# Optimization experiments

Hardware: AMD Instinct MI355X
Metric: run time of the kernel (lower is better)

Reference implementation:

```python
import jax, jax.numpy as jnp
import numpy as np

IN, HID, B = 512, 512, 16384

def _linear_params(key, fan_in, fan_out, bias_const=None):
    kw, kb = jax.random.split(key)
    bound = 1.0 / np.sqrt(fan_in)
    W = jax.random.uniform(kw, (fan_out, fan_in), jnp.float32, -bound, bound)
    if bias_const is None:
        b = jax.random.uniform(kb, (fan_out,), jnp.float32, -bound, bound)
    else:
        b = jnp.full((fan_out,), bias_const, jnp.float32)
    return W, b

def setup_inputs() -> dict:
    key = jax.random.key(0)
    ks = jax.random.split(key, 11)
    x = jax.random.normal(ks[0], (B, IN), jnp.float32)
    h = jax.random.normal(ks[1], (B, HID), jnp.float32)
    c = jax.random.normal(ks[2], (B, HID), jnp.float32)
    Wxi, bxi = _linear_params(ks[3], IN, HID)
    Wxo, bxo = _linear_params(ks[4], IN, HID)
    Wxf, bxf = _linear_params(ks[5], IN, HID, bias_const=1.0)
    Wxg, bxg = _linear_params(ks[6], IN, HID)
    Whi, bhi = _linear_params(ks[7], HID, HID)
    Who, bho = _linear_params(ks[8], HID, HID)
    Whf, bhf = _linear_params(ks[9], HID, HID, bias_const=1.0)
    Whg, bhg = _linear_params(ks[10], HID, HID)
    return dict(x=x, h=h, c=c,
                Wxi=Wxi, bxi=bxi, Wxo=Wxo, bxo=bxo, Wxf=Wxf, bxf=bxf, Wxg=Wxg, bxg=bxg,
                Whi=Whi, bhi=bhi, Who=Who, bho=bho, Whf=Whf, bhf=bhf, Whg=Whg, bhg=bhg)

def reference(x, h, c,
              Wxi, bxi, Wxo, bxo, Wxf, bxf, Wxg, bxg,
              Whi, bhi, Who, bho, Whf, bhf, Whg, bhg):
    # Batch the four input projections and four hidden projections into two GEMMs.
    Wx = jnp.concatenate([Wxi, Wxg, Wxf, Wxo], axis=0)   # [4H, IN]
    Wh = jnp.concatenate([Whi, Whg, Whf, Who], axis=0)   # [4H, HID]
    bx = jnp.concatenate([bxi, bxg, bxf, bxo], axis=0)
    bh = jnp.concatenate([bhi, bhg, bhf, bho], axis=0)
    gates = x @ Wx.T + h @ Wh.T + bx + bh                 # [B, 4H]
    i_pre, g_pre, f_pre, o_pre = jnp.split(gates, 4, axis=1)
    i = jax.nn.sigmoid(i_pre)
    g = jnp.tanh(g_pre)
    f = jax.nn.sigmoid(f_pre)
    o = jax.nn.sigmoid(o_pre)
    c_new = f * c + i * g
    h_new = o * jnp.tanh(c_new)
    return (h_new, c_new)
```

## Files before the change

kernel.cpp:

```cpp
#include <hip/hip_runtime.h>
#include <cstdint>
#include <cstddef>


#define BATCH 16384
#define KDIM  1024
#define NPK   2048
#define HIDN  512

#define BM 128
#define BN 128
#define BK 32

typedef __bf16 bf16x8 __attribute__((ext_vector_type(8)));
typedef float  f32x4  __attribute__((ext_vector_type(4)));

__device__ __forceinline__ unsigned short f2bf(float f) {
  unsigned int u = __builtin_bit_cast(unsigned int, f);
  u += 0x7fffu + ((u >> 16) & 1u);
  return (unsigned short)(u >> 16);
}

__device__ __forceinline__ float fast_sigmoid(float x) {
  return __builtin_amdgcn_rcpf(1.0f + __expf(-x));
}
__device__ __forceinline__ float fast_tanh(float x) {
  return 1.0f - 2.0f * __builtin_amdgcn_rcpf(1.0f + __expf(2.0f * x));
}

__device__ __forceinline__ void gload_lds16(const void* gp, void* lds_wave_base) {
  auto g = (const __attribute__((address_space(1))) unsigned int*)(unsigned long long)gp;
  auto l = (__attribute__((address_space(3))) unsigned int*)
           (unsigned int)(unsigned long long)lds_wave_base;
  __builtin_amdgcn_global_load_lds(g, l, 16, 0, 0);
}


__global__ __launch_bounds__(256) void pack_a(const float* __restrict__ x,
                                              const float* __restrict__ h,
                                              unsigned short* __restrict__ A) {
  int c = blockIdx.x * 256 + threadIdx.x;
  int idx = c << 3;
  int b = idx >> 10;
  int k = idx & 1023;
  const float* src = (k < 512) ? (x + b * 512 + k) : (h + b * 512 + (k - 512));
  float4 lo = ((const float4*)src)[0];
  float4 hi = ((const float4*)src)[1];
  union { unsigned short s[8]; uint4 u; } o;
  o.s[0]=f2bf(lo.x); o.s[1]=f2bf(lo.y); o.s[2]=f2bf(lo.z); o.s[3]=f2bf(lo.w);
  o.s[4]=f2bf(hi.x); o.s[5]=f2bf(hi.y); o.s[6]=f2bf(hi.z); o.s[7]=f2bf(hi.w);
  ((uint4*)A)[c] = o.u;
}

struct GatePtrs {
  const float* wx[4];
  const float* wh[4];
  const float* bx[4];
  const float* bh[4];
};

__global__ __launch_bounds__(256) void pack_w(GatePtrs P,
                                              unsigned short* __restrict__ W,
                                              float* __restrict__ bias) {
  int c = blockIdx.x * 256 + threadIdx.x;
  int r = c >> 7;
  int k = (c & 127) << 3;
  int b    = r >> 7;
  int rem  = r & 127;
  int wn   = (rem >> 6) & 1;
  int gate = (rem >> 4) & 3;
  int jl   = rem & 15;
  int j = b * 32 + wn * 16 + jl;
  const float* src = (k < 512) ? (P.wx[gate] + j * 512 + k)
                               : (P.wh[gate] + j * 512 + (k - 512));
  float4 lo = ((const float4*)src)[0];
  float4 hi = ((const float4*)src)[1];
  union { unsigned short s[8]; uint4 u; } o;
  o.s[0]=f2bf(lo.x); o.s[1]=f2bf(lo.y); o.s[2]=f2bf(lo.z); o.s[3]=f2bf(lo.w);
  o.s[4]=f2bf(hi.x); o.s[5]=f2bf(hi.y); o.s[6]=f2bf(hi.z); o.s[7]=f2bf(hi.w);
  ((uint4*)W)[c] = o.u;
  if ((c & 127) == 0) bias[r] = P.bx[gate][j] + P.bh[gate][j];
}


__global__ __launch_bounds__(256) void lstm_gemm(
    const unsigned short* __restrict__ A,
    const unsigned short* __restrict__ W,
    const float* __restrict__ bias,
    const float* __restrict__ Cin,
    float* __restrict__ Hout,
    float* __restrict__ Cout) {
  __shared__ __align__(16) unsigned short lds_a[BM * BK];
  __shared__ __align__(16) unsigned short lds_b[BN * BK];

  const int tid  = threadIdx.x;
  const int lane = tid & 63;
  const int wv   = tid >> 6;
  const int wm   = wv >> 1;
  const int wn   = wv & 1;
  const int bn   = blockIdx.x;
  const int bm   = blockIdx.y;

  const int srow = lane >> 2;
  const int scol = (lane & 3) << 3;
  const unsigned short* ga0 = A + (size_t)(bm * 128 + wv * 16 + srow) * KDIM + scol;
  const unsigned short* ga1 = A + (size_t)(bm * 128 + (wv + 4) * 16 + srow) * KDIM + scol;
  const unsigned short* gb0 = W + (size_t)(bn * 128 + wv * 16 + srow) * KDIM + scol;
  const unsigned short* gb1 = W + (size_t)(bn * 128 + (wv + 4) * 16 + srow) * KDIM + scol;
  unsigned short* la0 = lds_a + (wv * 16) * BK;
  unsigned short* la1 = lds_a + ((wv + 4) * 16) * BK;
  unsigned short* lb0 = lds_b + (wv * 16) * BK;
  unsigned short* lb1 = lds_b + ((wv + 4) * 16) * BK;

  f32x4 acc[4][4] = {};

  const int lrow = lane & 15;
  const int kg   = (lane >> 4) << 3;

  for (int kt = 0; kt < KDIM / BK; ++kt) {
    gload_lds16(ga0, la0);
    gload_lds16(ga1, la1);
    gload_lds16(gb0, lb0);
    gload_lds16(gb1, lb1);
    ga0 += BK; ga1 += BK; gb0 += BK; gb1 += BK;
    __syncthreads();

    bf16x8 af[4], bf[4];
#pragma unroll
    for (int mi = 0; mi < 4; ++mi)
      af[mi] = *reinterpret_cast<const bf16x8*>(
          &lds_a[(wm * 64 + mi * 16 + lrow) * BK + kg]);
#pragma unroll
    for (int ni = 0; ni < 4; ++ni)
      bf[ni] = *reinterpret_cast<const bf16x8*>(
          &lds_b[(wn * 64 + ni * 16 + lrow) * BK + kg]);
#pragma unroll
    for (int mi = 0; mi < 4; ++mi)
#pragma unroll
      for (int ni = 0; ni < 4; ++ni)
        acc[mi][ni] = __builtin_amdgcn_mfma_f32_16x16x32_bf16(
            af[mi], bf[ni], acc[mi][ni], 0, 0, 0);
    __syncthreads();
  }

  const int jl = lane & 15;
  const int j  = bn * 32 + wn * 16 + jl;
  const int rbase = bm * 128 + wm * 64 + ((lane >> 4) << 2);
  float bv[4];
#pragma unroll
  for (int ni = 0; ni < 4; ++ni)
    bv[ni] = bias[bn * 128 + wn * 64 + ni * 16 + jl];

#pragma unroll
  for (int mi = 0; mi < 4; ++mi) {
#pragma unroll
    for (int r = 0; r < 4; ++r) {
      int row = rbase + mi * 16 + r;
      float iv = fast_sigmoid(acc[mi][0][r] + bv[0]);
      float gv = fast_tanh   (acc[mi][1][r] + bv[1]);
      float fv = fast_sigmoid(acc[mi][2][r] + bv[2]);
      float ov = fast_sigmoid(acc[mi][3][r] + bv[3]);
      float cold = Cin[(size_t)row * HIDN + j];
      float cnew = fv * cold + iv * gv;
      Hout[(size_t)row * HIDN + j] = ov * fast_tanh(cnew);
      Cout[(size_t)row * HIDN + j] = cnew;
    }
  }
}


extern "C" void kernel_launch(void* const* d_in, const int* in_sizes, int n_in,
                              void* d_out, int out_size, void* d_ws, size_t ws_size,
                              hipStream_t stream) {
  const float* x   = (const float*)d_in[0];
  const float* h   = (const float*)d_in[1];
  const float* c   = (const float*)d_in[2];
  const float* Wxi = (const float*)d_in[3];  const float* bxi = (const float*)d_in[4];
  const float* Wxo = (const float*)d_in[5];  const float* bxo = (const float*)d_in[6];
  const float* Wxf = (const float*)d_in[7];  const float* bxf = (const float*)d_in[8];
  const float* Wxg = (const float*)d_in[9];  const float* bxg = (const float*)d_in[10];
  const float* Whi = (const float*)d_in[11]; const float* bhi = (const float*)d_in[12];
  const float* Who = (const float*)d_in[13]; const float* bho = (const float*)d_in[14];
  const float* Whf = (const float*)d_in[15]; const float* bhf = (const float*)d_in[16];
  const float* Whg = (const float*)d_in[17]; const float* bhg = (const float*)d_in[18];

  char* ws = (char*)d_ws;
  unsigned short* Apack = (unsigned short*)ws;
  unsigned short* Wpack = (unsigned short*)(ws + (size_t)BATCH * KDIM * 2);
  float* biasp = (float*)(ws + (size_t)BATCH * KDIM * 2 + (size_t)NPK * KDIM * 2);

  pack_a<<<(BATCH * KDIM / 8) / 256, 256, 0, stream>>>(x, h, Apack);

  GatePtrs P;
  P.wx[0] = Wxi; P.wx[1] = Wxg; P.wx[2] = Wxf; P.wx[3] = Wxo;
  P.wh[0] = Whi; P.wh[1] = Whg; P.wh[2] = Whf; P.wh[3] = Who;
  P.bx[0] = bxi; P.bx[1] = bxg; P.bx[2] = bxf; P.bx[3] = bxo;
  P.bh[0] = bhi; P.bh[1] = bhg; P.bh[2] = bhf; P.bh[3] = bho;
  pack_w<<<(NPK * KDIM / 8) / 256, 256, 0, stream>>>(P, Wpack, biasp);

  float* Hout = (float*)d_out;
  float* Cout = Hout + (size_t)BATCH * HIDN;
  dim3 grid(NPK / BN, BATCH / BM);
  lstm_gemm<<<grid, 256, 0, stream>>>(Apack, Wpack, biasp, c, Hout, Cout);
}
```

Baseline: 275.5 us.

## Fuse activation bf16 conversion into GEMM and swizzle LDS tiles

Drops the separate pack_a kernel. The GEMM now loads fp32 x and h tiles directly into LDS through global_load_lds and converts them to bf16 in registers before the MFMA. This removes a full pass that wrote and re-read the 32 MB bf16 A buffer. It also adds XOR/rotation swizzles to the A and B LDS layouts to reduce bank conflicts. In exchange, the A tile in LDS doubles in size, each block re-reads fp32 A (16 column blocks read it), and conversion work moves into the inner loop.

After: 313.9 us. 1.14x slower.

```diff
diff --git a/kernel.cpp b/kernel.cpp
--- a/kernel.cpp
+++ b/kernel.cpp
@@ -35,22 +35,6 @@
   __builtin_amdgcn_global_load_lds(g, l, 16, 0, 0);
 }
 
-
-__global__ __launch_bounds__(256) void pack_a(const float* __restrict__ x,
-                                              const float* __restrict__ h,
-                                              unsigned short* __restrict__ A) {
-  int c = blockIdx.x * 256 + threadIdx.x;
-  int idx = c << 3;
-  int b = idx >> 10;
-  int k = idx & 1023;
-  const float* src = (k < 512) ? (x + b * 512 + k) : (h + b * 512 + (k - 512));
-  float4 lo = ((const float4*)src)[0];
-  float4 hi = ((const float4*)src)[1];
-  union { unsigned short s[8]; uint4 u; } o;
-  o.s[0]=f2bf(lo.x); o.s[1]=f2bf(lo.y); o.s[2]=f2bf(lo.z); o.s[3]=f2bf(lo.w);
-  o.s[4]=f2bf(hi.x); o.s[5]=f2bf(hi.y); o.s[6]=f2bf(hi.z); o.s[7]=f2bf(hi.w);
-  ((uint4*)A)[c] = o.u;
-}
 
 struct GatePtrs {
   const float* wx[4];
@@ -84,13 +68,14 @@
 
 
 __global__ __launch_bounds__(256) void lstm_gemm(
-    const unsigned short* __restrict__ A,
+    const float* __restrict__ x,
+    const float* __restrict__ h,
     const unsigned short* __restrict__ W,
     const float* __restrict__ bias,
     const float* __restrict__ Cin,
     float* __restrict__ Hout,
     float* __restrict__ Cout) {
-  __shared__ __align__(16) unsigned short lds_a[BM * BK];
+  __shared__ __align__(16) float          lds_a[BM * BK];
   __shared__ __align__(16) unsigned short lds_b[BN * BK];
 
   const int tid  = threadIdx.x;
@@ -101,39 +86,58 @@
   const int bn   = blockIdx.x;
   const int bm   = blockIdx.y;
 
-  const int srow = lane >> 2;
-  const int scol = (lane & 3) << 3;
-  const unsigned short* ga0 = A + (size_t)(bm * 128 + wv * 16 + srow) * KDIM + scol;
-  const unsigned short* ga1 = A + (size_t)(bm * 128 + (wv + 4) * 16 + srow) * KDIM + scol;
-  const unsigned short* gb0 = W + (size_t)(bn * 128 + wv * 16 + srow) * KDIM + scol;
-  const unsigned short* gb1 = W + (size_t)(bn * 128 + (wv + 4) * 16 + srow) * KDIM + scol;
-  unsigned short* la0 = lds_a + (wv * 16) * BK;
-  unsigned short* la1 = lds_a + ((wv + 4) * 16) * BK;
-  unsigned short* lb0 = lds_b + (wv * 16) * BK;
-  unsigned short* lb1 = lds_b + ((wv + 4) * 16) * BK;
+  int offA[4];
+  float* ldsA[4];
+#pragma unroll
+  for (int t = 0; t < 4; ++t) {
+    int rloc = wv * 32 + t * 8 + (lane >> 3);
+    int q = ((lane & 7) - (lane >> 3)) & 7;
+    offA[t] = (bm * 128 + rloc) * 512 + q * 4;
+    ldsA[t] = lds_a + (wv * 32 + t * 8) * BK;
+  }
+  int offB[2];
+  unsigned short* ldsB[2];
+#pragma unroll
+  for (int t = 0; t < 2; ++t) {
+    int rloc = wv * 32 + t * 16 + (lane >> 2);
+    int q = (lane & 3) ^ ((lane >> 3) & 3);
+    offB[t] = (bn * 128 + rloc) * KDIM + q * 8;
+    ldsB[t] = lds_b + (wv * 32 + t * 16) * BK;
+  }
 
   f32x4 acc[4][4] = {};
 
   const int lrow = lane & 15;
-  const int kg   = (lane >> 4) << 3;
+  const int kq   = lane >> 4;
 
   for (int kt = 0; kt < KDIM / BK; ++kt) {
-    gload_lds16(ga0, la0);
-    gload_lds16(ga1, la1);
-    gload_lds16(gb0, lb0);
-    gload_lds16(gb1, lb1);
-    ga0 += BK; ga1 += BK; gb0 += BK; gb1 += BK;
+    const float* asrc = (kt < 16) ? x : h;
+    const int ak = (kt & 15) * BK;
+#pragma unroll
+    for (int t = 0; t < 4; ++t) gload_lds16(asrc + offA[t] + ak, ldsA[t]);
+#pragma unroll
+    for (int t = 0; t < 2; ++t) gload_lds16(W + offB[t] + kt * BK, ldsB[t]);
     __syncthreads();
 
     bf16x8 af[4], bf[4];
 #pragma unroll
-    for (int mi = 0; mi < 4; ++mi)
-      af[mi] = *reinterpret_cast<const bf16x8*>(
-          &lds_a[(wm * 64 + mi * 16 + lrow) * BK + kg]);
-#pragma unroll
-    for (int ni = 0; ni < 4; ++ni)
-      bf[ni] = *reinterpret_cast<const bf16x8*>(
-          &lds_b[(wn * 64 + ni * 16 + lrow) * BK + kg]);
+    for (int mi = 0; mi < 4; ++mi) {
+      int ra = wm * 64 + mi * 16 + lrow;
+      int c1 = (2 * kq + ra) & 7;
+      int c2 = (2 * kq + 1 + ra) & 7;
+      f32x4 a0 = *reinterpret_cast<const f32x4*>(&lds_a[ra * BK + c1 * 4]);
+      f32x4 a1 = *reinterpret_cast<const f32x4*>(&lds_a[ra * BK + c2 * 4]);
+      bf16x8 v;
+#pragma unroll
+      for (int e = 0; e < 4; ++e) { v[e] = (__bf16)a0[e]; v[e + 4] = (__bf16)a1[e]; }
+      af[mi] = v;
+    }
+#pragma unroll
+    for (int ni = 0; ni < 4; ++ni) {
+      int rn = wn * 64 + ni * 16 + lrow;
+      int cb = kq ^ ((lrow >> 1) & 3);
+      bf[ni] = *reinterpret_cast<const bf16x8*>(&lds_b[rn * BK + cb * 8]);
+    }
 #pragma unroll
     for (int mi = 0; mi < 4; ++mi)
 #pragma unroll
@@ -185,11 +189,8 @@
   const float* Whg = (const float*)d_in[17]; const float* bhg = (const float*)d_in[18];
 
   char* ws = (char*)d_ws;
-  unsigned short* Apack = (unsigned short*)ws;
-  unsigned short* Wpack = (unsigned short*)(ws + (size_t)BATCH * KDIM * 2);
-  float* biasp = (float*)(ws + (size_t)BATCH * KDIM * 2 + (size_t)NPK * KDIM * 2);
-
-  pack_a<<<(BATCH * KDIM / 8) / 256, 256, 0, stream>>>(x, h, Apack);
+  unsigned short* Wpack = (unsigned short*)ws;
+  float* biasp = (float*)(ws + (size_t)NPK * KDIM * 2);
 
   GatePtrs P;
   P.wx[0] = Wxi; P.wx[1] = Wxg; P.wx[2] = Wxf; P.wx[3] = Wxo;
@@ -201,5 +202,5 @@
   float* Hout = (float*)d_out;
   float* Cout = Hout + (size_t)BATCH * HIDN;
   dim3 grid(NPK / BN, BATCH / BM);
-  lstm_gemm<<<grid, 256, 0, stream>>>(Apack, Wpack, biasp, c, Hout, Cout);
-}
+  lstm_gemm<<<grid, 256, 0, stream>>>(x, h, Wpack, biasp, c, Hout, Cout);
+}
```

## Double-buffer LDS tiles to overlap global loads with MFMA compute

Applied to the files above, without the earlier changes.

Splits the A and B shared-memory tiles into two buffers and prefetches the next K tile into the spare buffer while the current one feeds the MFMAs. This drops one of the two barriers per K step. The aim is to hide global-to-LDS load latency behind matrix math. In exchange it doubles LDS use per block, which may lower occupancy. The compiler may also still insert conservative waits on the async LDS loads before the shared-memory reads, which would limit the overlap.

Result: faster. 266.6 us (-3.2%).

```diff
diff --git a/kernel.cpp b/kernel.cpp
--- a/kernel.cpp
+++ b/kernel.cpp
@@ -90,8 +90,8 @@
     const float* __restrict__ Cin,
     float* __restrict__ Hout,
     float* __restrict__ Cout) {
-  __shared__ __align__(16) unsigned short lds_a[BM * BK];
-  __shared__ __align__(16) unsigned short lds_b[BN * BK];
+  __shared__ __align__(16) unsigned short lds_a[2][BM * BK];
+  __shared__ __align__(16) unsigned short lds_b[2][BN * BK];
 
   const int tid  = threadIdx.x;
   const int lane = tid & 63;
@@ -107,40 +107,46 @@
   const unsigned short* ga1 = A + (size_t)(bm * 128 + (wv + 4) * 16 + srow) * KDIM + scol;
   const unsigned short* gb0 = W + (size_t)(bn * 128 + wv * 16 + srow) * KDIM + scol;
   const unsigned short* gb1 = W + (size_t)(bn * 128 + (wv + 4) * 16 + srow) * KDIM + scol;
-  unsigned short* la0 = lds_a + (wv * 16) * BK;
-  unsigned short* la1 = lds_a + ((wv + 4) * 16) * BK;
-  unsigned short* lb0 = lds_b + (wv * 16) * BK;
-  unsigned short* lb1 = lds_b + ((wv + 4) * 16) * BK;
+  const int la0 = (wv * 16) * BK;
+  const int la1 = ((wv + 4) * 16) * BK;
 
   f32x4 acc[4][4] = {};
 
   const int lrow = lane & 15;
   const int kg   = (lane >> 4) << 3;
 
+  gload_lds16(ga0, &lds_a[0][la0]);
+  gload_lds16(ga1, &lds_a[0][la1]);
+  gload_lds16(gb0, &lds_b[0][la0]);
+  gload_lds16(gb1, &lds_b[0][la1]);
+  ga0 += BK; ga1 += BK; gb0 += BK; gb1 += BK;
+
   for (int kt = 0; kt < KDIM / BK; ++kt) {
-    gload_lds16(ga0, la0);
-    gload_lds16(ga1, la1);
-    gload_lds16(gb0, lb0);
-    gload_lds16(gb1, lb1);
-    ga0 += BK; ga1 += BK; gb0 += BK; gb1 += BK;
+    const int cur = kt & 1;
     __syncthreads();
+    if (kt < KDIM / BK - 1) {
+      gload_lds16(ga0, &lds_a[cur ^ 1][la0]);
+      gload_lds16(ga1, &lds_a[cur ^ 1][la1]);
+      gload_lds16(gb0, &lds_b[cur ^ 1][la0]);
+      gload_lds16(gb1, &lds_b[cur ^ 1][la1]);
+      ga0 += BK; ga1 += BK; gb0 += BK; gb1 += BK;
+    }
 
     bf16x8 af[4], bf[4];
 #pragma unroll
     for (int mi = 0; mi < 4; ++mi)
       af[mi] = *reinterpret_cast<const bf16x8*>(
-          &lds_a[(wm * 64 + mi * 16 + lrow) * BK + kg]);
+          &lds_a[cur][(wm * 64 + mi * 16 + lrow) * BK + kg]);
 #pragma unroll
     for (int ni = 0; ni < 4; ++ni)
       bf[ni] = *reinterpret_cast<const bf16x8*>(
-          &lds_b[(wn * 64 + ni * 16 + lrow) * BK + kg]);
+          &lds_b[cur][(wn * 64 + ni * 16 + lrow) * BK + kg]);
 #pragma unroll
     for (int mi = 0; mi < 4; ++mi)
 #pragma unroll
       for (int ni = 0; ni < 4; ++ni)
         acc[mi][ni] = __builtin_amdgcn_mfma_f32_16x16x32_bf16(
             af[mi], bf[ni], acc[mi][ni], 0, 0, 0);
-    __syncthreads();
   }
 
   const int jl = lane & 15;
```

## Pack operands in MFMA fragment order and load directly to registers

Applied to the files above, without the earlier changes.

The pack kernels now write A and W in the exact per-lane MFMA fragment layout, so the GEMM loads bf16x8 fragments straight from global memory into registers and drops LDS staging and block barriers. Fragments are double-buffered in registers to prefetch the next K tile while the current MFMAs run. This removes LDS traffic and syncs but gives up LDS sharing between waves: each wave now reads its own fragments from global/L2, which duplicates reads across waves that share the same rows.

Result: slower. 284.3 us (+3.2%).

```diff
diff --git a/kernel.cpp b/kernel.cpp
--- a/kernel.cpp
+++ b/kernel.cpp
@@ -7,10 +7,7 @@
 #define KDIM  1024
 #define NPK   2048
 #define HIDN  512
-
-#define BM 128
-#define BN 128
-#define BK 32
+#define NKT   32
 
 typedef __bf16 bf16x8 __attribute__((ext_vector_type(8)));
 typedef float  f32x4  __attribute__((ext_vector_type(4)));
@@ -28,22 +25,18 @@
   return 1.0f - 2.0f * __builtin_amdgcn_rcpf(1.0f + __expf(2.0f * x));
 }
 
-__device__ __forceinline__ void gload_lds16(const void* gp, void* lds_wave_base) {
-  auto g = (const __attribute__((address_space(1))) unsigned int*)(unsigned long long)gp;
-  auto l = (__attribute__((address_space(3))) unsigned int*)
-           (unsigned int)(unsigned long long)lds_wave_base;
-  __builtin_amdgcn_global_load_lds(g, l, 16, 0, 0);
-}
-
-
-__global__ __launch_bounds__(256) void pack_a(const float* __restrict__ x,
-                                              const float* __restrict__ h,
-                                              unsigned short* __restrict__ A) {
+__global__ __launch_bounds__(256) void pack_a2(const float* __restrict__ x,
+                                               const float* __restrict__ h,
+                                               unsigned short* __restrict__ A) {
   int c = blockIdx.x * 256 + threadIdx.x;
-  int idx = c << 3;
-  int b = idx >> 10;
-  int k = idx & 1023;
-  const float* src = (k < 512) ? (x + b * 512 + k) : (h + b * 512 + (k - 512));
+  int lane = c & 63;
+  int g    = (c >> 6) & 7;
+  int kt   = (c >> 9) & 31;
+  int bm   = c >> 14;
+  int row  = bm * 128 + g * 16 + (lane & 15);
+  int col  = kt * 32 + ((lane >> 4) << 3);
+  const float* src = (col < 512) ? (x + (size_t)row * 512 + col)
+                                 : (h + (size_t)row * 512 + (col - 512));
   float4 lo = ((const float4*)src)[0];
   float4 hi = ((const float4*)src)[1];
   union { unsigned short s[8]; uint4 u; } o;
@@ -59,40 +52,38 @@
   const float* bh[4];
 };
 
-__global__ __launch_bounds__(256) void pack_w(GatePtrs P,
-                                              unsigned short* __restrict__ W,
-                                              float* __restrict__ bias) {
+__global__ __launch_bounds__(256) void pack_w2(GatePtrs P,
+                                               unsigned short* __restrict__ W,
+                                               float* __restrict__ bias) {
   int c = blockIdx.x * 256 + threadIdx.x;
-  int r = c >> 7;
-  int k = (c & 127) << 3;
-  int b    = r >> 7;
-  int rem  = r & 127;
-  int wn   = (rem >> 6) & 1;
-  int gate = (rem >> 4) & 3;
-  int jl   = rem & 15;
-  int j = b * 32 + wn * 16 + jl;
-  const float* src = (k < 512) ? (P.wx[gate] + j * 512 + k)
-                               : (P.wh[gate] + j * 512 + (k - 512));
+  int lane = c & 63;
+  int ni   = (c >> 6) & 3;
+  int wn   = (c >> 8) & 1;
+  int kt   = (c >> 9) & 31;
+  int bn   = c >> 14;
+  int jl   = lane & 15;
+  int j    = bn * 32 + wn * 16 + jl;
+  int col  = kt * 32 + ((lane >> 4) << 3);
+  const float* src = (col < 512) ? (P.wx[ni] + (size_t)j * 512 + col)
+                                 : (P.wh[ni] + (size_t)j * 512 + (col - 512));
   float4 lo = ((const float4*)src)[0];
   float4 hi = ((const float4*)src)[1];
   union { unsigned short s[8]; uint4 u; } o;
   o.s[0]=f2bf(lo.x); o.s[1]=f2bf(lo.y); o.s[2]=f2bf(lo.z); o.s[3]=f2bf(lo.w);
   o.s[4]=f2bf(hi.x); o.s[5]=f2bf(hi.y); o.s[6]=f2bf(hi.z); o.s[7]=f2bf(hi.w);
   ((uint4*)W)[c] = o.u;
-  if ((c & 127) == 0) bias[r] = P.bx[gate][j] + P.bh[gate][j];
+  if (kt == 0 && (lane >> 4) == 0)
+    bias[bn * 128 + wn * 64 + ni * 16 + jl] = P.bx[ni][j] + P.bh[ni][j];
 }
 
 
 __global__ __launch_bounds__(256) void lstm_gemm(
-    const unsigned short* __restrict__ A,
-    const unsigned short* __restrict__ W,
+    const bf16x8* __restrict__ Af,
+    const bf16x8* __restrict__ Bf,
     const float* __restrict__ bias,
     const float* __restrict__ Cin,
     float* __restrict__ Hout,
     float* __restrict__ Cout) {
-  __shared__ __align__(16) unsigned short lds_a[BM * BK];
-  __shared__ __align__(16) unsigned short lds_b[BN * BK];
-
   const int tid  = threadIdx.x;
   const int lane = tid & 63;
   const int wv   = tid >> 6;
@@ -101,46 +92,33 @@
   const int bn   = blockIdx.x;
   const int bm   = blockIdx.y;
 
-  const int srow = lane >> 2;
-  const int scol = (lane & 3) << 3;
-  const unsigned short* ga0 = A + (size_t)(bm * 128 + wv * 16 + srow) * KDIM + scol;
-  const unsigned short* ga1 = A + (size_t)(bm * 128 + (wv + 4) * 16 + srow) * KDIM + scol;
-  const unsigned short* gb0 = W + (size_t)(bn * 128 + wv * 16 + srow) * KDIM + scol;
-  const unsigned short* gb1 = W + (size_t)(bn * 128 + (wv + 4) * 16 + srow) * KDIM + scol;
-  unsigned short* la0 = lds_a + (wv * 16) * BK;
-  unsigned short* la1 = lds_a + ((wv + 4) * 16) * BK;
-  unsigned short* lb0 = lds_b + (wv * 16) * BK;
-  unsigned short* lb1 = lds_b + ((wv + 4) * 16) * BK;
+  const bf16x8* pa = Af + ((size_t)bm * 256 + wm * 4) * 64 + lane;
+  const bf16x8* pb = Bf + ((size_t)bn * 256 + wn * 4) * 64 + lane;
 
   f32x4 acc[4][4] = {};
+  bf16x8 fa[2][4], fb[2][4];
 
-  const int lrow = lane & 15;
-  const int kg   = (lane >> 4) << 3;
+#pragma unroll
+  for (int i = 0; i < 4; ++i) { fa[0][i] = pa[i * 64]; fb[0][i] = pb[i * 64]; }
 
-  for (int kt = 0; kt < KDIM / BK; ++kt) {
-    gload_lds16(ga0, la0);
-    gload_lds16(ga1, la1);
-    gload_lds16(gb0, lb0);
-    gload_lds16(gb1, lb1);
-    ga0 += BK; ga1 += BK; gb0 += BK; gb1 += BK;
-    __syncthreads();
-
-    bf16x8 af[4], bf[4];
 #pragma unroll
-    for (int mi = 0; mi < 4; ++mi)
-      af[mi] = *reinterpret_cast<const bf16x8*>(
-          &lds_a[(wm * 64 + mi * 16 + lrow) * BK + kg]);
+  for (int kt = 0; kt < NKT; ++kt) {
+    const int cur = kt & 1;
+    if (kt + 1 < NKT) {
+      const bf16x8* qa = pa + (kt + 1) * 512;
+      const bf16x8* qb = pb + (kt + 1) * 512;
 #pragma unroll
-    for (int ni = 0; ni < 4; ++ni)
-      bf[ni] = *reinterpret_cast<const bf16x8*>(
-          &lds_b[(wn * 64 + ni * 16 + lrow) * BK + kg]);
+      for (int i = 0; i < 4; ++i) {
+        fa[cur ^ 1][i] = qa[i * 64];
+        fb[cur ^ 1][i] = qb[i * 64];
+      }
+    }
 #pragma unroll
     for (int mi = 0; mi < 4; ++mi)
 #pragma unroll
       for (int ni = 0; ni < 4; ++ni)
         acc[mi][ni] = __builtin_amdgcn_mfma_f32_16x16x32_bf16(
-            af[mi], bf[ni], acc[mi][ni], 0, 0, 0);
-    __syncthreads();
+            fa[cur][mi], fb[cur][ni], acc[mi][ni], 0, 0, 0);
   }
 
   const int jl = lane & 15;
@@ -189,17 +167,18 @@
   unsigned short* Wpack = (unsigned short*)(ws + (size_t)BATCH * KDIM * 2);
   float* biasp = (float*)(ws + (size_t)BATCH * KDIM * 2 + (size_t)NPK * KDIM * 2);
 
-  pack_a<<<(BATCH * KDIM / 8) / 256, 256, 0, stream>>>(x, h, Apack);
+  pack_a2<<<(BATCH * KDIM / 8) / 256, 256, 0, stream>>>(x, h, Apack);
 
   GatePtrs P;
   P.wx[0] = Wxi; P.wx[1] = Wxg; P.wx[2] = Wxf; P.wx[3] = Wxo;
   P.wh[0] = Whi; P.wh[1] = Whg; P.wh[2] = Whf; P.wh[3] = Who;
   P.bx[0] = bxi; P.bx[1] = bxg; P.bx[2] = bxf; P.bx[3] = bxo;
   P.bh[0] = bhi; P.bh[1] = bhg; P.bh[2] = bhf; P.bh[3] = bho;
-  pack_w<<<(NPK * KDIM / 8) / 256, 256, 0, stream>>>(P, Wpack, biasp);
+  pack_w2<<<(NPK * KDIM / 8) / 256, 256, 0, stream>>>(P, Wpack, biasp);
 
   float* Hout = (float*)d_out;
   float* Cout = Hout + (size_t)BATCH * HIDN;
-  dim3 grid(NPK / BN, BATCH / BM);
-  lstm_gemm<<<grid, 256, 0, stream>>>(Apack, Wpack, biasp, c, Hout, Cout);
+  dim3 grid(NPK / 128, BATCH / 128);
+  lstm_gemm<<<grid, 256, 0, stream>>>((const bf16x8*)Apack, (const bf16x8*)Wpack,
+                                      biasp, c, Hout, Cout);
 }
```
